# Performance work log

Hardware: AMD Instinct MI355X
Metric: run time of the kernel (lower is better)

Reference implementation:

```python
import jax, jax.numpy as jnp
import numpy as np


def setup_inputs() -> dict:
    key = jax.random.key(0)
    ks = jax.random.split(key, 7)
    B, D, H, M, E = 8192, 512, 512, 50, 3
    return {
        "x": jax.random.normal(ks[0], (B, D), dtype=jnp.float32),
        "mem": jax.random.normal(ks[1], (M, D), dtype=jnp.float32),
        "routing_logits": jax.random.normal(ks[2], (E,), dtype=jnp.float32),
        "proj_W": jax.random.normal(ks[3], (H, D), dtype=jnp.float32) * 0.02,
        "proj_b": jax.random.normal(ks[4], (H,), dtype=jnp.float32) * 0.02,
        "ops_W": jax.random.normal(ks[5], (E, H, H), dtype=jnp.float32) * 0.02,
        "ops_b": jax.random.normal(ks[6], (E, H), dtype=jnp.float32) * 0.02,
    }


def reference(x, mem, routing_logits, proj_W, proj_b, ops_W, ops_b):
    # novelty: mean over (batch, memory) of L2 distance between x rows and memory rows
    diff = x[:, None, :] - mem[None, :, :]                 # [B, M, D] -- dominant memory traffic
    novelty = jnp.minimum(1.5, jnp.mean(jnp.linalg.norm(diff, axis=-1)))

    # top-2 routing over softmax of the (per-module, input-independent) logits
    weights = jax.nn.softmax(routing_logits)
    _, top2 = jax.lax.top_k(weights, 2)
    idx_a, idx_b = top2[0], top2[1]

    # operator = ReLU -> Linear(H, H) -> ReLU (torch Linear: y = x @ W.T + b)
    def op(h, W, b):
        return jax.nn.relu(jnp.einsum("bh,oh->bo", jax.nn.relu(h), W) + b)

    x_proj = jnp.einsum("bd,hd->bh", x, proj_W) + proj_b   # [B, H]
    x1 = op(x_proj, ops_W[idx_a], ops_b[idx_a])
    out = op(x1, ops_W[idx_b], ops_b[idx_b])
    return out, novelty
```

## Files before the change

kernel.cpp:

```cpp
#include <hip/hip_runtime.h>
#include <hip/hip_bf16.h>

typedef _Float16 f16;
typedef _Float16 f16x4 __attribute__((ext_vector_type(4)));
typedef _Float16 f16x8 __attribute__((ext_vector_type(8)));
typedef float f32x4 __attribute__((ext_vector_type(4)));

#define BD 512

__device__ __forceinline__ void llds16(const f16* g, f16* l) {
  __builtin_amdgcn_global_load_lds(
      (const __attribute__((address_space(1))) unsigned int*)g,
      (__attribute__((address_space(3))) unsigned int*)l,
      16, 0, 0);
}

__global__ __launch_bounds__(256, 2) void conv_nov_w_kernel(
    const float* __restrict__ x, const float* __restrict__ memf,
    const float* __restrict__ projW, const float* __restrict__ opsW,
    f16* __restrict__ wh, f16* __restrict__ xh,
    float* __restrict__ novPart) {
  __shared__ __align__(16) f16 memh[52 * BD];
  __shared__ __align__(16) f16 As[16 * BD];
  __shared__ float xn[16];
  __shared__ float red[4];
  const int t = threadIdx.x, l = t & 63, w = t >> 6;
  const int rbase = blockIdx.x * 16;

  #pragma unroll
  for (int i = 0; i < 25; ++i) {
    const int idx = i * 256 + t;
    const int row = idx >> 7;
    const int c4  = idx & 127;
    float4 v = ((const float4*)memf)[(size_t)row * 128 + c4];
    f16x4 h;
    h[0]=(f16)v.x; h[1]=(f16)v.y; h[2]=(f16)v.z; h[3]=(f16)v.w;
    const int ch = c4 >> 1;
    *(f16x4*)&memh[row * BD + (((ch ^ (row & 7)) << 3) | ((c4 & 1) << 2))] = h;
  }

  {
    const int e = (blockIdx.x * 256 + t) * 8;
    const float* s = (e < 262144) ? (projW + e) : (opsW + (e - 262144));
    float4 v0 = ((const float4*)s)[0];
    float4 v1 = ((const float4*)s)[1];
    f16x8 h;
    h[0]=(f16)v0.x; h[1]=(f16)v0.y; h[2]=(f16)v0.z; h[3]=(f16)v0.w;
    h[4]=(f16)v1.x; h[5]=(f16)v1.y; h[6]=(f16)v1.z; h[7]=(f16)v1.w;
    *(f16x8*)&wh[e] = h;
  }

  #pragma unroll
  for (int rr = 0; rr < 4; ++rr) {
    const int r = w * 4 + rr;
    const float* src = x + (size_t)(rbase + r) * BD + l * 8;
    float4 v0 = *(const float4*)src;
    float4 v1 = *(const float4*)(src + 4);
    f16x8 h;
    h[0]=(f16)v0.x; h[1]=(f16)v0.y; h[2]=(f16)v0.z; h[3]=(f16)v0.w;
    h[4]=(f16)v1.x; h[5]=(f16)v1.y; h[6]=(f16)v1.z; h[7]=(f16)v1.w;
    *(f16x8*)&xh[(size_t)(rbase + r) * BD + l * 8] = h;
    const int cs = l ^ (r & 7);
    *(f16x8*)&As[r * BD + cs * 8] = h;
    float ss = v0.x*v0.x + v0.y*v0.y + v0.z*v0.z + v0.w*v0.w
             + v1.x*v1.x + v1.y*v1.y + v1.z*v1.z + v1.w*v1.w;
    #pragma unroll
    for (int off = 32; off; off >>= 1) ss += __shfl_down(ss, off, 64);
    if (l == 0) xn[r] = ss;
  }
  __syncthreads();

  const int lr = l & 15, lk = l >> 4;
  if (w < 4) {
    const int mm = w * 16 + lr;
    const bool valid = (mm < 50);
    f32x4 acc = (f32x4){0.f, 0.f, 0.f, 0.f};
    float msq = 0.f;
    #pragma unroll
    for (int kk = 0; kk < BD; kk += 32) {
      const int ch = (kk >> 3) + lk;
      f16x8 bfr;
      if (valid) {
        bfr = *(const f16x8*)&memh[mm * BD + ((ch ^ (mm & 7)) << 3)];
        #pragma unroll
        for (int j = 0; j < 8; ++j) { float f = (float)bfr[j]; msq += f * f; }
      } else {
        #pragma unroll
        for (int j = 0; j < 8; ++j) bfr[j] = (f16)0.f;
      }
      f16x8 a = *(const f16x8*)&As[lr * BD + ((ch ^ (lr & 7)) << 3)];
      acc = __builtin_amdgcn_mfma_f32_16x16x32_f16(a, bfr, acc, 0, 0, 0);
    }
    msq += __shfl_xor(msq, 16, 64);
    msq += __shfl_xor(msq, 32, 64);
    float local = 0.f;
    if (valid) {
      #pragma unroll
      for (int j = 0; j < 4; ++j) {
        const int r0 = lk * 4 + j;
        float d = xn[r0] - 2.f * acc[j] + msq;
        local += sqrtf(fmaxf(d, 0.f));
      }
    }
    #pragma unroll
    for (int off = 32; off; off >>= 1) local += __shfl_down(local, off, 64);
    if (l == 0) red[w] = local;
  }
  __syncthreads();
  if (t == 0) novPart[blockIdx.x] = red[0] + red[1] + red[2] + red[3];
}

template <int PICK, int OUTF16>
__global__ __launch_bounds__(256, 2) void gemm_relu_kernel(
    const f16* __restrict__ A, const f16* __restrict__ Wall,
    const float* __restrict__ ball, const float* __restrict__ logits,
    void* __restrict__ Out, const float* __restrict__ novPart,
    float* __restrict__ novOut) {
  __shared__ __align__(16) char lds[4 * 16384];

  const int t = threadIdx.x;
  const int l = t & 63;
  const int w = t >> 6;
  const int wr = w >> 1, wc = w & 1;
  const int lr = l & 15, lk = l >> 4;

  if (PICK == 0 && blockIdx.x == 0 && blockIdx.y == 0 && w == 0) {
    float s = 0.f;
    #pragma unroll
    for (int i = 0; i < 8; ++i) s += novPart[l + i * 64];
    #pragma unroll
    for (int off = 32; off; off >>= 1) s += __shfl_down(s, off, 64);
    if (l == 0) novOut[0] = fminf(1.5f, s * (1.0f / (8192.0f * 50.0f)));
  }

  int widx = 0;
  if (PICK > 0) {
    float l0 = logits[0], l1 = logits[1], l2 = logits[2];
    int ia = 0; float ba = l0;
    if (l1 > ba) { ba = l1; ia = 1; }
    if (l2 > ba) { ba = l2; ia = 2; }
    if (PICK == 1) {
      widx = ia;
    } else {
      int ib = 0; float bb2 = -3.4e38f;
      if (ia != 0)             { bb2 = l0; ib = 0; }
      if (ia != 1 && l1 > bb2) { bb2 = l1; ib = 1; }
      if (ia != 2 && l2 > bb2) { bb2 = l2; ib = 2; }
      widx = ib;
    }
  }
  const f16* W = Wall + (size_t)widx * BD * BD;
  const float* bias = ball + widx * BD;

  const int rowBase = blockIdx.x * 64;
  const int colBase = blockIdx.y * 64;

  f32x4 acc[2][2];
  #pragma unroll
  for (int m = 0; m < 2; ++m)
    #pragma unroll
    for (int n = 0; n < 2; ++n) acc[m][n] = (f32x4){0.f, 0.f, 0.f, 0.f};

  auto stage = [&](int buf, int kt) {
    f16* Ab = (f16*)(lds + buf * 16384);
    f16* Bb = (f16*)(lds + buf * 16384 + 8192);
    #pragma unroll
    for (int i = 0; i < 2; ++i) {
      const int o = i * 4096 + t * 16;
      const int row = o >> 7;
      const int sch = ((o >> 4) & 7) ^ (row & 7);
      llds16(A + (size_t)(rowBase + row) * BD + kt + sch * 8,
             Ab + (i * 4096 + w * 1024) / 2);
      llds16(W + (size_t)(colBase + row) * BD + kt + sch * 8,
             Bb + (i * 4096 + w * 1024) / 2);
    }
  };

  auto compute = [&](int buf) {
    const f16* Ab = (const f16*)(lds + buf * 16384);
    const f16* Bb = (const f16*)(lds + buf * 16384 + 8192);
    #pragma unroll
    for (int kk = 0; kk < 64; kk += 32) {
      const int ch = (kk >> 3) + lk;
      f16x8 af[2], bf[2];
      #pragma unroll
      for (int m = 0; m < 2; ++m) {
        const int row = wr * 32 + m * 16 + lr;
        af[m] = *(const f16x8*)&Ab[row * 64 + ((ch ^ (row & 7)) << 3)];
      }
      #pragma unroll
      for (int n = 0; n < 2; ++n) {
        const int row = wc * 32 + n * 16 + lr;
        bf[n] = *(const f16x8*)&Bb[row * 64 + ((ch ^ (row & 7)) << 3)];
      }
      __builtin_amdgcn_s_setprio(1);
      #pragma unroll
      for (int m = 0; m < 2; ++m)
        #pragma unroll
        for (int n = 0; n < 2; ++n)
          acc[m][n] = __builtin_amdgcn_mfma_f32_16x16x32_f16(af[m], bf[n], acc[m][n], 0, 0, 0);
      __builtin_amdgcn_s_setprio(0);
    }
  };

  stage(0, 0);
  stage(1, 64);
  stage(2, 128);
  #pragma unroll
  for (int t8 = 0; t8 < 8; ++t8) {
    if (t8 < 6)       asm volatile("s_waitcnt vmcnt(8)" ::: "memory");
    else if (t8 == 6) asm volatile("s_waitcnt vmcnt(4)" ::: "memory");
    else              asm volatile("s_waitcnt vmcnt(0)" ::: "memory");
    __builtin_amdgcn_s_barrier();
    if (t8 < 5) stage((t8 + 3) & 3, (t8 + 3) * 64);
    compute(t8 & 3);
    asm volatile("s_waitcnt lgkmcnt(0)" ::: "memory");
  }

  #pragma unroll
  for (int n = 0; n < 2; ++n) {
    const int col = colBase + wc * 32 + n * 16 + lr;
    const float bbv = bias[col];
    #pragma unroll
    for (int m = 0; m < 2; ++m) {
      #pragma unroll
      for (int j = 0; j < 4; ++j) {
        const int rowg = rowBase + wr * 32 + m * 16 + lk * 4 + j;
        float v = fmaxf(acc[m][n][j] + bbv, 0.f);
        if (OUTF16) ((f16*)Out)[(size_t)rowg * BD + col] = (f16)v;
        else        ((float*)Out)[(size_t)rowg * BD + col] = v;
      }
    }
  }
}

extern "C" void kernel_launch(void* const* d_in, const int* in_sizes, int n_in,
                              void* d_out, int out_size, void* d_ws, size_t ws_size,
                              hipStream_t stream) {
  const float* x      = (const float*)d_in[0];
  const float* memf   = (const float*)d_in[1];
  const float* logits = (const float*)d_in[2];
  const float* projW  = (const float*)d_in[3];
  const float* projB  = (const float*)d_in[4];
  const float* opsW   = (const float*)d_in[5];
  const float* opsB   = (const float*)d_in[6];
  float* out = (float*)d_out;

  char* ws = (char*)d_ws;
  f16*   xh      = (f16*)(ws);
  f16*   g0      = (f16*)(ws + 8388608);
  f16*   wh      = (f16*)(ws + 16777216);
  float* novPart = (float*)(ws + 18874368);

  conv_nov_w_kernel<<<512, 256, 0, stream>>>(x, memf, projW, opsW, wh, xh, novPart);

  gemm_relu_kernel<0, 1><<<dim3(128, 8), 256, 0, stream>>>(
      xh, wh, projB, logits, (void*)g0, novPart, out + 4194304);
  gemm_relu_kernel<1, 1><<<dim3(128, 8), 256, 0, stream>>>(
      g0, wh + 262144, opsB, logits, (void*)xh, novPart, out + 4194304);
  gemm_relu_kernel<2, 0><<<dim3(128, 8), 256, 0, stream>>>(
      xh, wh + 262144, opsB, logits, (void*)out, novPart, out + 4194304);
}
```

Baseline: 45.66 us.

## Split conversion and novelty into separate streaming and MFMA kernels

The fused convert+novelty kernel is split in two. A simple streaming kernel converts x and the weights to fp16 across 2560 blocks. A novelty kernel then loads fp16 x into LDS with global_load_lds and handles 32 rows per block using all 8 waves, where before only 4 waves did MFMA work. The aim is a higher-bandwidth conversion pass and less repeated per-block conversion of mem (256 blocks instead of 512). The cost is an extra launch and a re-read of xh, and x norms are now computed from fp16-rounded values.

```diff
diff --git a/kernel.cpp b/kernel.cpp
--- a/kernel.cpp
+++ b/kernel.cpp
@@ -15,18 +15,48 @@
       16, 0, 0);
 }
 
-__global__ __launch_bounds__(256, 2) void conv_nov_w_kernel(
-    const float* __restrict__ x, const float* __restrict__ memf,
-    const float* __restrict__ projW, const float* __restrict__ opsW,
-    f16* __restrict__ wh, f16* __restrict__ xh,
+__global__ __launch_bounds__(256) void stream_cvt_kernel(
+    const float* __restrict__ x, const float* __restrict__ projW,
+    const float* __restrict__ opsW, f16* __restrict__ xh, f16* __restrict__ wh) {
+  const int bid = blockIdx.x, t = threadIdx.x;
+  const float* src;
+  f16* dst;
+  if (bid < 2048) {
+    const int e = (bid * 256 + t) * 8;
+    src = x + e; dst = xh + e;
+  } else {
+    const int e = ((bid - 2048) * 256 + t) * 8;
+    src = (e < 262144) ? (projW + e) : (opsW + (e - 262144));
+    dst = wh + e;
+  }
+  float4 v0 = ((const float4*)src)[0];
+  float4 v1 = ((const float4*)src)[1];
+  f16x8 h;
+  h[0]=(f16)v0.x; h[1]=(f16)v0.y; h[2]=(f16)v0.z; h[3]=(f16)v0.w;
+  h[4]=(f16)v1.x; h[5]=(f16)v1.y; h[6]=(f16)v1.z; h[7]=(f16)v1.w;
+  *(f16x8*)dst = h;
+}
+
+__global__ __launch_bounds__(256, 1) void novelty_kernel(
+    const f16* __restrict__ xh, const float* __restrict__ memf,
     float* __restrict__ novPart) {
-  __shared__ __align__(16) f16 memh[52 * BD];
-  __shared__ __align__(16) f16 As[16 * BD];
-  __shared__ float xn[16];
-  __shared__ float red[4];
+  __shared__ __align__(16) f16 As[32 * BD];
+  __shared__ __align__(16) f16 memh[50 * BD];
+  __shared__ float xn[32];
+  __shared__ float red[8];
   const int t = threadIdx.x, l = t & 63, w = t >> 6;
-  const int rbase = blockIdx.x * 16;
-
+  const int lr = l & 15, lk = l >> 4;
+  const int rbase = blockIdx.x * 32;
+
+  #pragma unroll
+  for (int i = 0; i < 8; ++i) {
+    const int o = i * 4096 + t * 16;
+    const int row = o >> 10;
+    const int p = (o >> 4) & 63;
+    const int sch = p ^ (row & 7);
+    llds16(xh + (size_t)(rbase + row) * BD + sch * 8,
+           As + (i * 4096 + w * 1024) / 2);
+  }
   #pragma unroll
   for (int i = 0; i < 25; ++i) {
     const int idx = i * 256 + t;
@@ -38,76 +68,64 @@
     const int ch = c4 >> 1;
     *(f16x4*)&memh[row * BD + (((ch ^ (row & 7)) << 3) | ((c4 & 1) << 2))] = h;
   }
+  __syncthreads();
 
   {
-    const int e = (blockIdx.x * 256 + t) * 8;
-    const float* s = (e < 262144) ? (projW + e) : (opsW + (e - 262144));
-    float4 v0 = ((const float4*)s)[0];
-    float4 v1 = ((const float4*)s)[1];
-    f16x8 h;
-    h[0]=(f16)v0.x; h[1]=(f16)v0.y; h[2]=(f16)v0.z; h[3]=(f16)v0.w;
-    h[4]=(f16)v1.x; h[5]=(f16)v1.y; h[6]=(f16)v1.z; h[7]=(f16)v1.w;
-    *(f16x8*)&wh[e] = h;
-  }
-
-  #pragma unroll
-  for (int rr = 0; rr < 4; ++rr) {
-    const int r = w * 4 + rr;
-    const float* src = x + (size_t)(rbase + r) * BD + l * 8;
-    float4 v0 = *(const float4*)src;
-    float4 v1 = *(const float4*)(src + 4);
-    f16x8 h;
-    h[0]=(f16)v0.x; h[1]=(f16)v0.y; h[2]=(f16)v0.z; h[3]=(f16)v0.w;
-    h[4]=(f16)v1.x; h[5]=(f16)v1.y; h[6]=(f16)v1.z; h[7]=(f16)v1.w;
-    *(f16x8*)&xh[(size_t)(rbase + r) * BD + l * 8] = h;
-    const int cs = l ^ (r & 7);
-    *(f16x8*)&As[r * BD + cs * 8] = h;
-    float ss = v0.x*v0.x + v0.y*v0.y + v0.z*v0.z + v0.w*v0.w
-             + v1.x*v1.x + v1.y*v1.y + v1.z*v1.z + v1.w*v1.w;
-    #pragma unroll
-    for (int off = 32; off; off >>= 1) ss += __shfl_down(ss, off, 64);
-    if (l == 0) xn[r] = ss;
+    const int row = t >> 3, sub = t & 7;
+    float ss = 0.f;
+    #pragma unroll
+    for (int q = 0; q < 8; ++q) {
+      f16x8 a = *(const f16x8*)&As[row * BD + (sub * 8 + q) * 8];
+      #pragma unroll
+      for (int j = 0; j < 8; ++j) { float f = (float)a[j]; ss += f * f; }
+    }
+    ss += __shfl_xor(ss, 1, 64); ss += __shfl_xor(ss, 2, 64); ss += __shfl_xor(ss, 4, 64);
+    if (sub == 0) xn[row] = ss;
   }
   __syncthreads();
 
-  const int lr = l & 15, lk = l >> 4;
-  if (w < 4) {
-    const int mm = w * 16 + lr;
-    const bool valid = (mm < 50);
-    f32x4 acc = (f32x4){0.f, 0.f, 0.f, 0.f};
-    float msq = 0.f;
-    #pragma unroll
-    for (int kk = 0; kk < BD; kk += 32) {
-      const int ch = (kk >> 3) + lk;
-      f16x8 bfr;
-      if (valid) {
-        bfr = *(const f16x8*)&memh[mm * BD + ((ch ^ (mm & 7)) << 3)];
-        #pragma unroll
-        for (int j = 0; j < 8; ++j) { float f = (float)bfr[j]; msq += f * f; }
-      } else {
-        #pragma unroll
-        for (int j = 0; j < 8; ++j) bfr[j] = (f16)0.f;
-      }
-      f16x8 a = *(const f16x8*)&As[lr * BD + ((ch ^ (lr & 7)) << 3)];
-      acc = __builtin_amdgcn_mfma_f32_16x16x32_f16(a, bfr, acc, 0, 0, 0);
-    }
-    msq += __shfl_xor(msq, 16, 64);
-    msq += __shfl_xor(msq, 32, 64);
-    float local = 0.f;
+  const int mg = w & 3, xh2 = w >> 2;
+  const int mm = mg * 16 + lr;
+  const bool valid = (mm < 50);
+  f32x4 acc = (f32x4){0.f, 0.f, 0.f, 0.f};
+  float msq = 0.f;
+  #pragma unroll
+  for (int kk = 0; kk < BD; kk += 32) {
+    const int ch = (kk >> 3) + lk;
+    f16x8 bfr;
     if (valid) {
-      #pragma unroll
-      for (int j = 0; j < 4; ++j) {
-        const int r0 = lk * 4 + j;
-        float d = xn[r0] - 2.f * acc[j] + msq;
-        local += sqrtf(fmaxf(d, 0.f));
-      }
-    }
-    #pragma unroll
-    for (int off = 32; off; off >>= 1) local += __shfl_down(local, off, 64);
-    if (l == 0) red[w] = local;
-  }
+      bfr = *(const f16x8*)&memh[mm * BD + ((ch ^ (mm & 7)) << 3)];
+      #pragma unroll
+      for (int j = 0; j < 8; ++j) { float f = (float)bfr[j]; msq += f * f; }
+    } else {
+      #pragma unroll
+      for (int j = 0; j < 8; ++j) bfr[j] = (f16)0.f;
+    }
+    const int arow = xh2 * 16 + lr;
+    f16x8 a = *(const f16x8*)&As[arow * BD + ((ch ^ (lr & 7)) << 3)];
+    acc = __builtin_amdgcn_mfma_f32_16x16x32_f16(a, bfr, acc, 0, 0, 0);
+  }
+  msq += __shfl_xor(msq, 16, 64);
+  msq += __shfl_xor(msq, 32, 64);
+  float local = 0.f;
+  if (valid) {
+    #pragma unroll
+    for (int j = 0; j < 4; ++j) {
+      const int r0 = xh2 * 16 + lk * 4 + j;
+      float d = xn[r0] - 2.f * acc[j] + msq;
+      local += sqrtf(fmaxf(d, 0.f));
+    }
+  }
+  #pragma unroll
+  for (int off = 32; off; off >>= 1) local += __shfl_down(local, off, 64);
+  if (l == 0) red[w] = local;
   __syncthreads();
-  if (t == 0) novPart[blockIdx.x] = red[0] + red[1] + red[2] + red[3];
+  if (t == 0) {
+    float s = 0.f;
+    #pragma unroll
+    for (int i = 0; i < 8; ++i) s += red[i];
+    novPart[blockIdx.x] = s;
+  }
 }
 
 template <int PICK, int OUTF16>
@@ -125,9 +143,7 @@
   const int lr = l & 15, lk = l >> 4;
 
   if (PICK == 0 && blockIdx.x == 0 && blockIdx.y == 0 && w == 0) {
-    float s = 0.f;
-    #pragma unroll
-    for (int i = 0; i < 8; ++i) s += novPart[l + i * 64];
+    float s = novPart[l] + novPart[l + 64] + novPart[l + 128] + novPart[l + 192];
     #pragma unroll
     for (int off = 32; off; off >>= 1) s += __shfl_down(s, off, 64);
     if (l == 0) novOut[0] = fminf(1.5f, s * (1.0f / (8192.0f * 50.0f)));
@@ -252,7 +268,8 @@
   f16*   wh      = (f16*)(ws + 16777216);
   float* novPart = (float*)(ws + 18874368);
 
-  conv_nov_w_kernel<<<512, 256, 0, stream>>>(x, memf, projW, opsW, wh, xh, novPart);
+  stream_cvt_kernel<<<2560, 256, 0, stream>>>(x, projW, opsW, xh, wh);
+  novelty_kernel<<<256, 256, 0, stream>>>(xh, memf, novPart);
 
   gemm_relu_kernel<0, 1><<<dim3(128, 8), 256, 0, stream>>>(
       xh, wh, projB, logits, (void*)g0, novPart, out + 4194304);
```

Result: slower. 49.81 us (+9.1%).

## Fuse x conversion and novelty computation into first projection GEMM

Applied to the files above, without the earlier changes.

Replaces the conversion/novelty kernel with a small prep kernel that converts only the weights and the memory bank to fp16. The first GEMM now loads fp32 x directly into LDS through a triple-buffered pipeline and converts it while building fragments. Blocks in column 0 also compute the novelty distances against the padded memory bank in the same loop. This removes the fp16 copy of x and its extra write and read pass, at the cost of more LDS per block and a heavier inner loop for the novelty blocks.

```diff
diff --git a/kernel.cpp b/kernel.cpp
--- a/kernel.cpp
+++ b/kernel.cpp
@@ -1,113 +1,200 @@
 #include <hip/hip_runtime.h>
-#include <hip/hip_bf16.h>
 
 typedef _Float16 f16;
-typedef _Float16 f16x4 __attribute__((ext_vector_type(4)));
 typedef _Float16 f16x8 __attribute__((ext_vector_type(8)));
 typedef float f32x4 __attribute__((ext_vector_type(4)));
 
 #define BD 512
 
-__device__ __forceinline__ void llds16(const f16* g, f16* l) {
+__device__ __forceinline__ void llds16(const void* g, void* l) {
   __builtin_amdgcn_global_load_lds(
       (const __attribute__((address_space(1))) unsigned int*)g,
       (__attribute__((address_space(3))) unsigned int*)l,
       16, 0, 0);
 }
-
-__global__ __launch_bounds__(256, 2) void conv_nov_w_kernel(
-    const float* __restrict__ x, const float* __restrict__ memf,
+__device__ __forceinline__ f16x8 cvt8(float4 a, float4 b) {
+  f16x8 h;
+  h[0]=(f16)a.x; h[1]=(f16)a.y; h[2]=(f16)a.z; h[3]=(f16)a.w;
+  h[4]=(f16)b.x; h[5]=(f16)b.y; h[6]=(f16)b.z; h[7]=(f16)b.w;
+  return h;
+}
+
+__global__ __launch_bounds__(256) void prep_kernel(
     const float* __restrict__ projW, const float* __restrict__ opsW,
-    f16* __restrict__ wh, f16* __restrict__ xh,
-    float* __restrict__ novPart) {
-  __shared__ __align__(16) f16 memh[52 * BD];
-  __shared__ __align__(16) f16 As[16 * BD];
-  __shared__ float xn[16];
-  __shared__ float red[4];
-  const int t = threadIdx.x, l = t & 63, w = t >> 6;
-  const int rbase = blockIdx.x * 16;
-
-  #pragma unroll
-  for (int i = 0; i < 25; ++i) {
-    const int idx = i * 256 + t;
-    const int row = idx >> 7;
-    const int c4  = idx & 127;
-    float4 v = ((const float4*)memf)[(size_t)row * 128 + c4];
-    f16x4 h;
-    h[0]=(f16)v.x; h[1]=(f16)v.y; h[2]=(f16)v.z; h[3]=(f16)v.w;
-    const int ch = c4 >> 1;
-    *(f16x4*)&memh[row * BD + (((ch ^ (row & 7)) << 3) | ((c4 & 1) << 2))] = h;
-  }
-
-  {
-    const int e = (blockIdx.x * 256 + t) * 8;
+    const float* __restrict__ memf, f16* __restrict__ wh,
+    f16* __restrict__ memh) {
+  const int bid = blockIdx.x, t = threadIdx.x;
+  if (bid < 512) {
+    const int e = (bid * 256 + t) * 8;
     const float* s = (e < 262144) ? (projW + e) : (opsW + (e - 262144));
     float4 v0 = ((const float4*)s)[0];
     float4 v1 = ((const float4*)s)[1];
+    *(f16x8*)&wh[e] = cvt8(v0, v1);
+  } else {
+    const int e = ((bid - 512) * 256 + t) * 8;
+    const int row = e >> 9;
     f16x8 h;
-    h[0]=(f16)v0.x; h[1]=(f16)v0.y; h[2]=(f16)v0.z; h[3]=(f16)v0.w;
-    h[4]=(f16)v1.x; h[5]=(f16)v1.y; h[6]=(f16)v1.z; h[7]=(f16)v1.w;
-    *(f16x8*)&wh[e] = h;
-  }
-
-  #pragma unroll
-  for (int rr = 0; rr < 4; ++rr) {
-    const int r = w * 4 + rr;
-    const float* src = x + (size_t)(rbase + r) * BD + l * 8;
-    float4 v0 = *(const float4*)src;
-    float4 v1 = *(const float4*)(src + 4);
-    f16x8 h;
-    h[0]=(f16)v0.x; h[1]=(f16)v0.y; h[2]=(f16)v0.z; h[3]=(f16)v0.w;
-    h[4]=(f16)v1.x; h[5]=(f16)v1.y; h[6]=(f16)v1.z; h[7]=(f16)v1.w;
-    *(f16x8*)&xh[(size_t)(rbase + r) * BD + l * 8] = h;
-    const int cs = l ^ (r & 7);
-    *(f16x8*)&As[r * BD + cs * 8] = h;
-    float ss = v0.x*v0.x + v0.y*v0.y + v0.z*v0.z + v0.w*v0.w
-             + v1.x*v1.x + v1.y*v1.y + v1.z*v1.z + v1.w*v1.w;
-    #pragma unroll
-    for (int off = 32; off; off >>= 1) ss += __shfl_down(ss, off, 64);
-    if (l == 0) xn[r] = ss;
-  }
-  __syncthreads();
-
+    if (row < 50) {
+      float4 v0 = ((const float4*)(memf + e))[0];
+      float4 v1 = ((const float4*)(memf + e))[1];
+      h = cvt8(v0, v1);
+    } else {
+      #pragma unroll
+      for (int j = 0; j < 8; ++j) h[j] = (f16)0.f;
+    }
+    *(f16x8*)&memh[e] = h;
+  }
+}
+
+__global__ __launch_bounds__(256, 2) void gemm1_nov_kernel(
+    const float* __restrict__ x, const f16* __restrict__ wh,
+    const f16* __restrict__ memh, const float* __restrict__ projB,
+    f16* __restrict__ g0, float* __restrict__ novPart) {
+  __shared__ __align__(16) char lds[3 * 16384];
+  __shared__ float red[4];
+
+  const int t = threadIdx.x, l = t & 63, w = t >> 6;
+  const int wr = w >> 1, wc = w & 1;
   const int lr = l & 15, lk = l >> 4;
-  if (w < 4) {
-    const int mm = w * 16 + lr;
-    const bool valid = (mm < 50);
-    f32x4 acc = (f32x4){0.f, 0.f, 0.f, 0.f};
-    float msq = 0.f;
-    #pragma unroll
-    for (int kk = 0; kk < BD; kk += 32) {
-      const int ch = (kk >> 3) + lk;
-      f16x8 bfr;
-      if (valid) {
-        bfr = *(const f16x8*)&memh[mm * BD + ((ch ^ (mm & 7)) << 3)];
+  const int rowBase = blockIdx.x * 64, colBase = blockIdx.y * 64;
+  const bool NOV = (blockIdx.y == 0);
+
+  const int aRow = (t * 16) >> 7;
+  const int aCh  = ((t * 16) >> 4) & 7;
+  const int bRow = (t * 16) >> 6;
+  const int bCh  = ((t * 16) >> 4) & 3;
+
+  auto stage = [&](int buf, int kt) {
+    char* base = lds + buf * 16384;
+    #pragma unroll
+    for (int i = 0; i < 2; ++i) {
+      const int row = aRow + i * 32;
+      llds16(x + (size_t)(rowBase + row) * BD + kt + ((aCh ^ (row & 7)) * 4),
+             base + i * 4096 + w * 1024);
+    }
+    llds16(wh + (size_t)(colBase + bRow) * BD + kt + ((bCh ^ (bRow & 3)) * 8),
+           base + 8192 + w * 1024);
+    if (NOV)
+      llds16(memh + (size_t)bRow * BD + kt + ((bCh ^ (bRow & 3)) * 8),
+             base + 12288 + w * 1024);
+  };
+
+  f32x4 acc[2][2], nacc[4];
+  #pragma unroll
+  for (int m = 0; m < 2; ++m)
+    #pragma unroll
+    for (int n = 0; n < 2; ++n) acc[m][n] = (f32x4){0.f,0.f,0.f,0.f};
+  #pragma unroll
+  for (int q = 0; q < 4; ++q) nacc[q] = (f32x4){0.f,0.f,0.f,0.f};
+  float xsq[4] = {0.f, 0.f, 0.f, 0.f};
+  float msq = 0.f;
+
+  auto readA = [&](const float* Ab, int r) -> f16x8 {
+    float4 r0 = *(const float4*)&Ab[r * 32 + (((2 * lk) ^ (r & 7)) << 2)];
+    float4 r1 = *(const float4*)&Ab[r * 32 + (((2 * lk + 1) ^ (r & 7)) << 2)];
+    return cvt8(r0, r1);
+  };
+
+  auto compute = [&](int buf) {
+    const float* Ab = (const float*)(lds + buf * 16384);
+    const f16* Bb = (const f16*)(lds + buf * 16384 + 8192);
+    const f16* Mb = (const f16*)(lds + buf * 16384 + 12288);
+    f16x8 af[2], bf[2];
+    #pragma unroll
+    for (int m = 0; m < 2; ++m) af[m] = readA(Ab, wr * 32 + m * 16 + lr);
+    #pragma unroll
+    for (int n = 0; n < 2; ++n) {
+      const int row = wc * 32 + n * 16 + lr;
+      bf[n] = *(const f16x8*)&Bb[row * 32 + ((lk ^ (row & 3)) << 3)];
+    }
+    __builtin_amdgcn_s_setprio(1);
+    #pragma unroll
+    for (int m = 0; m < 2; ++m)
+      #pragma unroll
+      for (int n = 0; n < 2; ++n)
+        acc[m][n] = __builtin_amdgcn_mfma_f32_16x16x32_f16(af[m], bf[n], acc[m][n], 0, 0, 0);
+    __builtin_amdgcn_s_setprio(0);
+    if (NOV) {
+      const int mrow = w * 16 + lr;
+      f16x8 mf = *(const f16x8*)&Mb[mrow * 32 + ((lk ^ (mrow & 3)) << 3)];
+      #pragma unroll
+      for (int j = 0; j < 8; ++j) { float f = (float)mf[j]; msq += f * f; }
+      f16x8 aq[4];
+      if (wr == 0) {
+        aq[0] = af[0]; aq[1] = af[1];
+        aq[2] = readA(Ab, 32 + lr); aq[3] = readA(Ab, 48 + lr);
+      } else {
+        aq[0] = readA(Ab, lr); aq[1] = readA(Ab, 16 + lr);
+        aq[2] = af[0]; aq[3] = af[1];
+      }
+      #pragma unroll
+      for (int q = 0; q < 4; ++q) {
         #pragma unroll
-        for (int j = 0; j < 8; ++j) { float f = (float)bfr[j]; msq += f * f; }
-      } else {
-        #pragma unroll
-        for (int j = 0; j < 8; ++j) bfr[j] = (f16)0.f;
-      }
-      f16x8 a = *(const f16x8*)&As[lr * BD + ((ch ^ (lr & 7)) << 3)];
-      acc = __builtin_amdgcn_mfma_f32_16x16x32_f16(a, bfr, acc, 0, 0, 0);
-    }
+        for (int j = 0; j < 8; ++j) { float f = (float)aq[q][j]; xsq[q] += f * f; }
+        nacc[q] = __builtin_amdgcn_mfma_f32_16x16x32_f16(aq[q], mf, nacc[q], 0, 0, 0);
+      }
+    }
+  };
+
+  stage(0, 0);
+  stage(1, 32);
+  #pragma unroll
+  for (int tt = 0; tt < 16; ++tt) {
+    if (NOV) {
+      if (tt < 15) asm volatile("s_waitcnt vmcnt(4)" ::: "memory");
+      else         asm volatile("s_waitcnt vmcnt(0)" ::: "memory");
+    } else {
+      if (tt < 15) asm volatile("s_waitcnt vmcnt(3)" ::: "memory");
+      else         asm volatile("s_waitcnt vmcnt(0)" ::: "memory");
+    }
+    __builtin_amdgcn_s_barrier();
+    if (tt < 14) stage((tt + 2) % 3, (tt + 2) * 32);
+    compute(tt % 3);
+    asm volatile("s_waitcnt lgkmcnt(0)" ::: "memory");
+  }
+
+  if (NOV) {
     msq += __shfl_xor(msq, 16, 64);
     msq += __shfl_xor(msq, 32, 64);
+    #pragma unroll
+    for (int q = 0; q < 4; ++q) {
+      xsq[q] += __shfl_xor(xsq[q], 16, 64);
+      xsq[q] += __shfl_xor(xsq[q], 32, 64);
+    }
+    const int mm = w * 16 + lr;
     float local = 0.f;
-    if (valid) {
+    if (mm < 50) {
       #pragma unroll
       for (int j = 0; j < 4; ++j) {
-        const int r0 = lk * 4 + j;
-        float d = xn[r0] - 2.f * acc[j] + msq;
-        local += sqrtf(fmaxf(d, 0.f));
+        const int r16 = lk * 4 + j;
+        #pragma unroll
+        for (int q = 0; q < 4; ++q) {
+          const float xs = __shfl(xsq[q], r16, 64);
+          float d = xs - 2.f * nacc[q][j] + msq;
+          local += sqrtf(fmaxf(d, 0.f));
+        }
       }
     }
     #pragma unroll
     for (int off = 32; off; off >>= 1) local += __shfl_down(local, off, 64);
     if (l == 0) red[w] = local;
-  }
-  __syncthreads();
-  if (t == 0) novPart[blockIdx.x] = red[0] + red[1] + red[2] + red[3];
+    __syncthreads();
+    if (t == 0) novPart[blockIdx.x] = red[0] + red[1] + red[2] + red[3];
+  }
+
+  #pragma unroll
+  for (int n = 0; n < 2; ++n) {
+    const int col = colBase + wc * 32 + n * 16 + lr;
+    const float bbv = projB[col];
+    #pragma unroll
+    for (int m = 0; m < 2; ++m) {
+      #pragma unroll
+      for (int j = 0; j < 4; ++j) {
+        const int rowg = rowBase + wr * 32 + m * 16 + lk * 4 + j;
+        g0[(size_t)rowg * BD + col] = (f16)fmaxf(acc[m][n][j] + bbv, 0.f);
+      }
+    }
+  }
 }
 
 template <int PICK, int OUTF16>
@@ -124,30 +211,26 @@
   const int wr = w >> 1, wc = w & 1;
   const int lr = l & 15, lk = l >> 4;
 
-  if (PICK == 0 && blockIdx.x == 0 && blockIdx.y == 0 && w == 0) {
-    float s = 0.f;
-    #pragma unroll
-    for (int i = 0; i < 8; ++i) s += novPart[l + i * 64];
+  if (PICK == 2 && blockIdx.x == 0 && blockIdx.y == 0 && w == 0) {
+    float s = novPart[l] + novPart[l + 64];
     #pragma unroll
     for (int off = 32; off; off >>= 1) s += __shfl_down(s, off, 64);
     if (l == 0) novOut[0] = fminf(1.5f, s * (1.0f / (8192.0f * 50.0f)));
   }
 
-  int widx = 0;
-  if (PICK > 0) {
-    float l0 = logits[0], l1 = logits[1], l2 = logits[2];
-    int ia = 0; float ba = l0;
-    if (l1 > ba) { ba = l1; ia = 1; }
-    if (l2 > ba) { ba = l2; ia = 2; }
-    if (PICK == 1) {
-      widx = ia;
-    } else {
-      int ib = 0; float bb2 = -3.4e38f;
-      if (ia != 0)             { bb2 = l0; ib = 0; }
-      if (ia != 1 && l1 > bb2) { bb2 = l1; ib = 1; }
-      if (ia != 2 && l2 > bb2) { bb2 = l2; ib = 2; }
-      widx = ib;
-    }
+  float l0 = logits[0], l1 = logits[1], l2 = logits[2];
+  int ia = 0; float ba = l0;
+  if (l1 > ba) { ba = l1; ia = 1; }
+  if (l2 > ba) { ba = l2; ia = 2; }
+  int widx;
+  if (PICK == 1) {
+    widx = ia;
+  } else {
+    int ib = 0; float bb2 = -3.4e38f;
+    if (ia != 0)             { bb2 = l0; ib = 0; }
+    if (ia != 1 && l1 > bb2) { bb2 = l1; ib = 1; }
+    if (ia != 2 && l2 > bb2) { bb2 = l2; ib = 2; }
+    widx = ib;
   }
   const f16* W = Wall + (size_t)widx * BD * BD;
   const float* bias = ball + widx * BD;
@@ -170,9 +253,9 @@
       const int row = o >> 7;
       const int sch = ((o >> 4) & 7) ^ (row & 7);
       llds16(A + (size_t)(rowBase + row) * BD + kt + sch * 8,
-             Ab + (i * 4096 + w * 1024) / 2);
+             (char*)Ab + i * 4096 + w * 1024);
       llds16(W + (size_t)(colBase + row) * BD + kt + sch * 8,
-             Bb + (i * 4096 + w * 1024) / 2);
+             (char*)Bb + i * 4096 + w * 1024);
     }
   };
 
@@ -247,17 +330,17 @@
   float* out = (float*)d_out;
 
   char* ws = (char*)d_ws;
-  f16*   xh      = (f16*)(ws);
-  f16*   g0      = (f16*)(ws + 8388608);
+  f16*   g0      = (f16*)(ws);
+  f16*   h1      = (f16*)(ws + 8388608);
   f16*   wh      = (f16*)(ws + 16777216);
-  float* novPart = (float*)(ws + 18874368);
-
-  conv_nov_w_kernel<<<512, 256, 0, stream>>>(x, memf, projW, opsW, wh, xh, novPart);
-
-  gemm_relu_kernel<0, 1><<<dim3(128, 8), 256, 0, stream>>>(
-      xh, wh, projB, logits, (void*)g0, novPart, out + 4194304);
+  f16*   memh    = (f16*)(ws + 18874368);
+  float* novPart = (float*)(ws + 18939904);
+
+  prep_kernel<<<528, 256, 0, stream>>>(projW, opsW, memf, wh, memh);
+
+  gemm1_nov_kernel<<<dim3(128, 8), 256, 0, stream>>>(x, wh, memh, projB, g0, novPart);
   gemm_relu_kernel<1, 1><<<dim3(128, 8), 256, 0, stream>>>(
-      g0, wh + 262144, opsB, logits, (void*)xh, novPart, out + 4194304);
+      g0, wh + 262144, opsB, logits, (void*)h1, novPart, out + 4194304);
   gemm_relu_kernel<2, 0><<<dim3(128, 8), 256, 0, stream>>>(
-      xh, wh + 262144, opsB, logits, (void*)out, novPart, out + 4194304);
-}
+      h1, wh + 262144, opsB, logits, (void*)out, novPart, out + 4194304);
+}
```

Measured after the change: 48.38 us. 6.0% more time.
